# Optimization experiments

Hardware: AMD Instinct MI355X
Metric: run time of the kernel (lower is better)

The kernel has to match this reference:

```python
import jax, jax.numpy as jnp
import numpy as np
import math

D_MODEL = 1024
N_HEADS = 16
Q_PROJ = D_MODEL // 4
KV_PROJ = D_MODEL // 4
DH = D_MODEL // N_HEADS
LN_EPS = 1e-5


def _layernorm(x, gamma, beta):
    mu = jnp.mean(x, axis=-1, keepdims=True)
    var = jnp.mean(jnp.square(x - mu), axis=-1, keepdims=True)
    return (x - mu) * jax.lax.rsqrt(var + LN_EPS) * gamma + beta


def setup_inputs() -> dict:
    key = jax.random.key(0)
    ks = jax.random.split(key, 7)
    B, S = 2, 2048
    x = jax.random.normal(ks[0], (B, S, D_MODEL), dtype=jnp.float32)
    W_dq = 0.01 * jax.random.normal(ks[1], (D_MODEL, Q_PROJ), dtype=jnp.float32)
    W_uq = 0.01 * jax.random.normal(ks[2], (Q_PROJ, D_MODEL), dtype=jnp.float32)
    W_dkv = 0.01 * jax.random.normal(ks[3], (D_MODEL, KV_PROJ), dtype=jnp.float32)
    W_ukv = 0.01 * jax.random.normal(ks[4], (KV_PROJ, 2 * D_MODEL), dtype=jnp.float32)
    W_o = 0.01 * jax.random.normal(ks[5], (D_MODEL, D_MODEL), dtype=jnp.float32)
    return {
        "x": x,
        "W_dq": W_dq, "W_uq": W_uq,
        "q_ln_g": jnp.ones((Q_PROJ,), jnp.float32), "q_ln_b": jnp.zeros((Q_PROJ,), jnp.float32),
        "W_dkv": W_dkv, "W_ukv": W_ukv,
        "kv_ln_g": jnp.ones((KV_PROJ,), jnp.float32), "kv_ln_b": jnp.zeros((KV_PROJ,), jnp.float32),
        "W_o": W_o,
    }


def reference(x, W_dq, W_uq, q_ln_g, q_ln_b, W_dkv, W_ukv, kv_ln_g, kv_ln_b, W_o):
    B, S, D = x.shape
    # low-rank Q path
    cq = _layernorm(x @ W_dq, q_ln_g, q_ln_b)          # [B,S,q_proj]
    Q = cq @ W_uq                                       # [B,S,D]
    # low-rank KV path
    ckv = _layernorm(x @ W_dkv, kv_ln_g, kv_ln_b)       # [B,S,kv_proj]
    KV = ckv @ W_ukv                                    # [B,S,2D]
    K, V = KV[..., :D], KV[..., D:]
    q = Q.reshape(B, S, N_HEADS, DH)
    k = K.reshape(B, S, N_HEADS, DH)
    v = V.reshape(B, S, N_HEADS, DH)
    scores = jnp.einsum("bqhd,bkhd->bhqk", q, k) / math.sqrt(float(DH))
    # faithful to original: multiply by tril mask, then set exact zeros to -inf
    mask = jnp.tril(jnp.ones((S, S), dtype=scores.dtype))
    scores = scores * mask
    scores = jnp.where(scores == 0, -jnp.inf, scores)
    attn = jax.nn.softmax(scores, axis=-1)
    out = jnp.einsum("bhqk,bkhd->bqhd", attn, v).reshape(B, S, D)
    return out @ W_o.T
```

## Files before the change

kernel.cpp:

```cpp
#include <hip/hip_runtime.h>

typedef __bf16 bf16;
typedef __bf16 bf16x4 __attribute__((ext_vector_type(4)));
typedef __bf16 bf16x8 __attribute__((ext_vector_type(8)));
typedef float f32x4 __attribute__((ext_vector_type(4)));

#define D_MODEL 1024
#define PROJ    256
#define SEQ     2048
#define BATCH   2
#define TOK     4096
#define NH      16
#define DH      64
#define NEG_BIG (-1e30f)
#define QSCALE  0.18033688011112042f

#if __has_builtin(__builtin_amdgcn_exp2f)
#define EXP2(x) __builtin_amdgcn_exp2f(x)
#else
#define EXP2(x) exp2f(x)
#endif

typedef __attribute__((address_space(3))) unsigned int  lds_u32;
typedef __attribute__((address_space(1))) unsigned int  glb_u32;

__device__ __forceinline__ void gl2lds16(const void* gsrc, void* ldst) {
    __builtin_amdgcn_global_load_lds((const glb_u32*)gsrc, (lds_u32*)ldst, 16, 0, 0);
}

template <int CTRL>
__device__ __forceinline__ float dppmov(float x) {
    int i = __builtin_bit_cast(int, x);
    i = __builtin_amdgcn_update_dpp(i, i, CTRL, 0xf, 0xf, false);
    return __builtin_bit_cast(float, i);
}
__device__ __forceinline__ float rowsum16(float v) {
    v += dppmov<0xB1>(v);
    v += dppmov<0x4E>(v);
    v += dppmov<0x141>(v);
    v += dppmov<0x140>(v);
    return v;
}

__global__ __launch_bounds__(256) void prep_weights_kernel(
    const float* __restrict__ W_o, const float* __restrict__ x,
    bf16* __restrict__ Wo16, bf16* __restrict__ x16) {
    const int R0 = 1048576;
    const int R1 = R0 + 4194304;
    for (int i = blockIdx.x * blockDim.x + threadIdx.x; i < R1;
         i += gridDim.x * blockDim.x) {
        if (i < R0) Wo16[i] = (bf16)W_o[i];
        else        x16[i - R0] = (bf16)x[i - R0];
    }
}

__global__ __launch_bounds__(256) void transpose_cvt_kernel(
    const float* __restrict__ W_dq, const float* __restrict__ W_dkv,
    const float* __restrict__ W_uq, const float* __restrict__ W_ukv,
    bf16* __restrict__ Wt_dq, bf16* __restrict__ Wt_dkv,
    bf16* __restrict__ Wt_uq, bf16* __restrict__ Wt_ukv) {
    __shared__ float tile[64][65];
    const int m = blockIdx.y;
    const float* src; bf16* dst; int R, C;
    if (m == 0)      { src = W_dq;  dst = Wt_dq;  R = 1024; C = 256; }
    else if (m == 1) { src = W_dkv; dst = Wt_dkv; R = 1024; C = 256; }
    else if (m == 2) { src = W_uq;  dst = Wt_uq;  R = 256;  C = 1024; }
    else             { src = W_ukv; dst = Wt_ukv; R = 256;  C = 2048; }
    const int tilesC = C >> 6;
    const int ntile = (R >> 6) * tilesC;
    const int t = blockIdx.x;
    if (t >= ntile) return;
    const int r0 = (t / tilesC) << 6;
    const int c0 = (t % tilesC) << 6;
    const int tr = threadIdx.x >> 6;
    const int tc = threadIdx.x & 63;
#pragma unroll
    for (int i = 0; i < 16; ++i)
        tile[tr * 16 + i][tc] = src[(size_t)(r0 + tr * 16 + i) * C + c0 + tc];
    __syncthreads();
#pragma unroll
    for (int i = 0; i < 16; ++i)
        dst[(size_t)(c0 + tr * 16 + i) * R + r0 + tc] = (bf16)tile[tc][tr * 16 + i];
}

__global__ __launch_bounds__(256) void gemm_ln_kernel(
    const bf16* __restrict__ x16,
    const bf16* __restrict__ Wt_q, const bf16* __restrict__ Wt_kv,
    const float* __restrict__ q_g, const float* __restrict__ q_b,
    const float* __restrict__ kv_g, const float* __restrict__ kv_b,
    bf16* __restrict__ cq, bf16* __restrict__ ckv) {
    __shared__ alignas(16) bf16 xA[2][16 * 32];
    __shared__ alignas(16) bf16 wB[2][256 * 32];
    __shared__ float red1[4][16];
    __shared__ float red2[4][16];

    const int K = 1024;
    const bf16* Wt = blockIdx.y ? Wt_kv : Wt_q;
    const float* gamma = blockIdx.y ? kv_g : q_g;
    const float* beta  = blockIdx.y ? kv_b : q_b;
    bf16* out = blockIdx.y ? ckv : cq;

    const int m0 = blockIdx.x * 16;
    const int wv = threadIdx.x >> 6;
    const int lane = threadIdx.x & 63;
    const int g = lane >> 4;
    const int ln16 = lane & 15;

    const int crow = lane >> 2;
    const int ckc = lane & 3;
    const bf16* gx = x16 + (size_t)(m0 + crow) * K + ckc * 8;
    const bf16* gw = Wt + (size_t)(64 * wv + crow) * K + ckc * 8;

    f32x4 acc[4] = {};

    if (wv == 0) gl2lds16(gx, (char*)xA);
#pragma unroll
    for (int i = 0; i < 4; ++i)
        gl2lds16(gw + (size_t)i * 16 * K, (char*)wB + wv * 4096 + i * 1024);
    __syncthreads();

    int buf = 0;
    for (int k0 = 0; k0 < K; k0 += 32) {
        if (k0 + 32 < K) {
            const int nb = buf ^ 1;
            if (wv == 0) gl2lds16(gx + k0 + 32, (char*)xA + nb * 1024);
#pragma unroll
            for (int i = 0; i < 4; ++i)
                gl2lds16(gw + (size_t)i * 16 * K + k0 + 32,
                         (char*)wB + nb * 16384 + wv * 4096 + i * 1024);
        }
        const bf16* cx = &xA[buf][0];
        const bf16* cw = &wB[buf][0];
        bf16x8 a = *(const bf16x8*)(cx + ln16 * 32 + g * 8);
#pragma unroll
        for (int t = 0; t < 4; ++t) {
            bf16x8 b = *(const bf16x8*)(cw + (wv * 64 + 16 * t + ln16) * 32 + g * 8);
            acc[t] = __builtin_amdgcn_mfma_f32_16x16x32_bf16(a, b, acc[t], 0, 0, 0);
        }
        __syncthreads();
        buf ^= 1;
    }

    float s1[4], s2[4];
#pragma unroll
    for (int r = 0; r < 4; ++r) {
        float a = 0.f, b = 0.f;
#pragma unroll
        for (int t = 0; t < 4; ++t) { float v = acc[t][r]; a += v; b += v * v; }
        s1[r] = rowsum16(a); s2[r] = rowsum16(b);
    }
    if (ln16 == 0) {
#pragma unroll
        for (int r = 0; r < 4; ++r) {
            red1[wv][g * 4 + r] = s1[r];
            red2[wv][g * 4 + r] = s2[r];
        }
    }
    __syncthreads();
#pragma unroll
    for (int r = 0; r < 4; ++r) {
        int rl = g * 4 + r;
        float t1 = red1[0][rl] + red1[1][rl] + red1[2][rl] + red1[3][rl];
        float t2 = red2[0][rl] + red2[1][rl] + red2[2][rl] + red2[3][rl];
        float mu = t1 * (1.0f / 256.0f);
        float var = t2 * (1.0f / 256.0f) - mu * mu;
        float rs = rsqrtf(var + 1e-5f);
        int row = m0 + rl;
#pragma unroll
        for (int t = 0; t < 4; ++t) {
            int col = wv * 64 + 16 * t + ln16;
            float v = (acc[t][r] - mu) * rs * gamma[col] + beta[col];
            out[(size_t)row * PROJ + col] = (bf16)v;
        }
    }
}

template <typename OutT>
__device__ __forceinline__ void gemm_body(
    const bf16* __restrict__ A, const bf16* __restrict__ Bt,
    OutT* __restrict__ C, bf16* __restrict__ C2, int N, int K,
    int bx, int by, int mode, bf16* tA, bf16* tB) {
    const int w = threadIdx.x >> 6;
    const int lane = threadIdx.x & 63;
    const int g = lane >> 4;
    const int ln16 = lane & 15;
    const int wr = w >> 1;
    const int wc = w & 1;

    const int m0 = bx * 64;
    const int n0 = by * 128;

    const int crow = lane >> 2;
    const int ckc = lane & 3;
    const bf16* gA  = A  + (size_t)(m0 + w * 16 + crow) * K + ckc * 8;
    const bf16* gB0 = Bt + (size_t)(n0 + w * 16 + crow) * K + ckc * 8;
    const bf16* gB1 = Bt + (size_t)(n0 + 64 + w * 16 + crow) * K + ckc * 8;

    f32x4 acc[2][4] = {};

    gl2lds16(gA, (char*)tA + w * 1024);
    gl2lds16(gB0, (char*)tB + w * 1024);
    gl2lds16(gB1, (char*)tB + 4096 + w * 1024);
    __syncthreads();

    int buf = 0;
    for (int k0 = 0; k0 < K; k0 += 32) {
        if (k0 + 32 < K) {
            const int nb = buf ^ 1;
            gl2lds16(gA + k0 + 32, (char*)tA + nb * 4096 + w * 1024);
            gl2lds16(gB0 + k0 + 32, (char*)tB + nb * 8192 + w * 1024);
            gl2lds16(gB1 + k0 + 32, (char*)tB + nb * 8192 + 4096 + w * 1024);
        }
        const bf16* cA = tA + buf * 2048;
        const bf16* cB = tB + buf * 4096;

        bf16x8 af[2], bfr[4];
#pragma unroll
        for (int s = 0; s < 2; ++s)
            af[s] = *(const bf16x8*)(cA + (wr * 32 + s * 16 + ln16) * 32 + g * 8);
#pragma unroll
        for (int t = 0; t < 4; ++t)
            bfr[t] = *(const bf16x8*)(cB + (wc * 64 + t * 16 + ln16) * 32 + g * 8);
#pragma unroll
        for (int s = 0; s < 2; ++s)
#pragma unroll
            for (int t = 0; t < 4; ++t)
                acc[s][t] = __builtin_amdgcn_mfma_f32_16x16x32_bf16(
                    af[s], bfr[t], acc[s][t], 0, 0, 0);
        __syncthreads();
        buf ^= 1;
    }

#pragma unroll
    for (int s = 0; s < 2; ++s)
#pragma unroll
        for (int t = 0; t < 4; ++t) {
            const int col = n0 + wc * 64 + t * 16 + ln16;
            const int tok0 = m0 + wr * 32 + s * 16 + g * 4;
            if (mode == 2 && col >= 1024) {
                int cc = col - 1024;
                int h = cc >> 6, d = cc & 63;
                int b = tok0 >> 11, sq = tok0 & 2047;
                bf16x4 pk;
#pragma unroll
                for (int r = 0; r < 4; ++r) pk[r] = (bf16)acc[s][t][r];
                *(bf16x4*)(C2 + ((size_t)((b * 16 + h) * 64 + d) * SEQ + sq)) = pk;
            } else {
#pragma unroll
                for (int r = 0; r < 4; ++r) {
                    int row = tok0 + r;
                    float v = acc[s][t][r];
                    if (mode == 0) {
                        C[(size_t)row * N + col] = (OutT)v;
                    } else {
                        if (mode == 1) v *= QSCALE;
                        int h = col >> 6, d = col & 63;
                        int b = row >> 11, sq = row & 2047;
                        C[((size_t)((b * 16 + h) * 2048 + sq)) * 64 + d] = (OutT)v;
                    }
                }
            }
        }
}

__global__ __launch_bounds__(256) void gemm_o_kernel(
    const bf16* __restrict__ A, const bf16* __restrict__ Bt,
    float* __restrict__ C, int M, int N, int K) {
    __shared__ alignas(16) bf16 tA[2][64 * 32];
    __shared__ alignas(16) bf16 tB[2][128 * 32];
    gemm_body<float>(A, Bt, C, nullptr, N, K, blockIdx.x, blockIdx.y, 0,
                     &tA[0][0], &tB[0][0]);
}

__global__ __launch_bounds__(256) void gemm_qkv_kernel(
    const bf16* __restrict__ cq, const bf16* __restrict__ Wt_uq,
    const bf16* __restrict__ ckv, const bf16* __restrict__ Wt_ukv,
    bf16* __restrict__ Qh, bf16* __restrict__ Kh, bf16* __restrict__ Vt) {
    __shared__ alignas(16) bf16 tA[2][64 * 32];
    __shared__ alignas(16) bf16 tB[2][128 * 32];
    const int i = blockIdx.x;
    if (i < 512) {
        gemm_body<bf16>(cq, Wt_uq, Qh, nullptr, D_MODEL, PROJ,
                        i >> 3, i & 7, 1, &tA[0][0], &tB[0][0]);
    } else {
        const int j = i - 512;
        gemm_body<bf16>(ckv, Wt_ukv, Kh, Vt, 2 * D_MODEL, PROJ,
                        j >> 4, j & 15, 2, &tA[0][0], &tB[0][0]);
    }
}

__device__ __forceinline__ void qk_exp_pack(
    int k0, int q, bool masked, int g, int ln16,
    bf16x8 aq0, bf16x8 aq1, const bf16x8* Kf,
    bf16x8& P1, bf16x8& P2) {
    f32x4 sc[4];
    __builtin_amdgcn_s_setprio(1);
#pragma unroll
    for (int c = 0; c < 4; ++c) {
        f32x4 z = {};
        z = __builtin_amdgcn_mfma_f32_16x16x32_bf16(Kf[2 * c], aq0, z, 0, 0, 0);
        z = __builtin_amdgcn_mfma_f32_16x16x32_bf16(Kf[2 * c + 1], aq1, z, 0, 0, 0);
        sc[c] = z;
    }
    __builtin_amdgcn_s_setprio(0);
    if (masked) {
        const int kb = k0 + 8 * g;
#pragma unroll
        for (int c = 0; c < 4; ++c)
#pragma unroll
            for (int r = 0; r < 4; ++r) {
                int kcol = kb + (c & 1) * 4 + r + ((c >> 1) << 5);
                if (kcol > q) sc[c][r] = NEG_BIG;
            }
    }
#pragma unroll
    for (int c = 0; c < 4; ++c)
#pragma unroll
        for (int r = 0; r < 4; ++r) sc[c][r] = EXP2(sc[c][r]);
#pragma unroll
    for (int r = 0; r < 4; ++r) {
        P1[r] = (bf16)sc[0][r]; P1[4 + r] = (bf16)sc[1][r];
        P2[r] = (bf16)sc[2][r]; P2[4 + r] = (bf16)sc[3][r];
    }
}

__device__ __forceinline__ void pv_accum(
    bf16x8 P1, bf16x8 P2, const bf16x8* Vf, bf16x8 vones,
    f32x4* o, f32x4& oli) {
    __builtin_amdgcn_s_setprio(1);
#pragma unroll
    for (int t = 0; t < 4; ++t) {
        o[t] = __builtin_amdgcn_mfma_f32_16x16x32_bf16(Vf[2 * t], P1, o[t], 0, 0, 0);
        o[t] = __builtin_amdgcn_mfma_f32_16x16x32_bf16(Vf[2 * t + 1], P2, o[t], 0, 0, 0);
    }
    oli = __builtin_amdgcn_mfma_f32_16x16x32_bf16(vones, P1, oli, 0, 0, 0);
    oli = __builtin_amdgcn_mfma_f32_16x16x32_bf16(vones, P2, oli, 0, 0, 0);
    __builtin_amdgcn_s_setprio(0);
}

__global__ __launch_bounds__(256) void attn_kernel(
    const bf16* __restrict__ Qh, const bf16* __restrict__ Kh,
    const bf16* __restrict__ Vt, bf16* __restrict__ AT) {
    __shared__ alignas(128) bf16 kbuf[2][64 * 64];
    __shared__ alignas(128) bf16 vbuf[2][64 * 64];

    const int lane = threadIdx.x & 63;
    const int g = lane >> 4;
    const int ln16 = lane & 15;
    const int wv = threadIdx.x >> 6;

    const int bh = blockIdx.x & 31;
    const int qsuper = 31 - (blockIdx.x >> 5);
    const int nt = qsuper + 1;
    const int qb = qsuper * 64 + wv * 16;
    const int q = qb + ln16;

    const bf16* Kbh = Kh + (size_t)bh * SEQ * DH;
    const bf16* Vbh = Vt + (size_t)bh * DH * SEQ;

    const int rho = lane >> 3;
    const int sl  = lane & 7;
    int kofs[2];
    size_t vofs[2];
#pragma unroll
    for (int i = 0; i < 2; ++i) {
        const int row = 16 * wv + 8 * i + rho;
        const int c = sl ^ ((rho & 3) | ((i & 1) << 2));
        kofs[i] = row * 64 + c * 8;
        vofs[i] = (size_t)row * SEQ + c * 8;
    }

    const int row_base = ((ln16 & 12) << 1) + (ln16 & 3);
    int kro[4], vro[4];
#pragma unroll
    for (int c = 0; c < 4; ++c) {
        const int row = row_base + (c & 1) * 4 + ((c >> 1) << 5);
        const int fr = (row & 3) | (((row >> 3) & 1) << 2);
        kro[c] = row * 128 + (g ^ fr) * 16;
    }
#pragma unroll
    for (int t = 0; t < 4; ++t) {
        const int d = 16 * t + ln16;
        const int fd = (d & 3) | (((d >> 3) & 1) << 2);
        vro[t] = d * 128 + (g ^ fd) * 16;
    }

    const bf16* qp = Qh + ((size_t)bh * SEQ + q) * DH + g * 8;
    bf16x8 aq0 = *(const bf16x8*)qp, aq1 = *(const bf16x8*)(qp + 32);

    bf16x8 vones;
#pragma unroll
    for (int i = 0; i < 8; ++i) vones[i] = (bf16)1.0f;

    f32x4 o[4] = {};
    f32x4 oli = {};

#pragma unroll
    for (int i = 0; i < 2; ++i) {
        gl2lds16(Kbh + kofs[i], (char*)kbuf + wv * 2048 + i * 1024);
        gl2lds16(Vbh + vofs[i], (char*)vbuf + wv * 2048 + i * 1024);
    }
    __syncthreads();

    int cur = 0;
    for (int kt = 0; kt < nt; ++kt) {
        if (kt + 1 < nt) {
            const size_t k0n = (size_t)(kt + 1) * 64;
            char* kb = (char*)kbuf + (cur ^ 1) * 8192 + wv * 2048;
            char* vb = (char*)vbuf + (cur ^ 1) * 8192 + wv * 2048;
#pragma unroll
            for (int i = 0; i < 2; ++i) {
                gl2lds16(Kbh + k0n * 64 + kofs[i], kb + i * 1024);
                gl2lds16(Vbh + vofs[i] + k0n, vb + i * 1024);
            }
        }

        const char* kb = (const char*)kbuf + cur * 8192;
        const char* vb = (const char*)vbuf + cur * 8192;
        bf16x8 Kf[8], Vf[8];
#pragma unroll
        for (int c = 0; c < 4; ++c) {
            Kf[2 * c]     = *(const bf16x8*)(kb + kro[c]);
            Kf[2 * c + 1] = *(const bf16x8*)(kb + (kro[c] ^ 64));
        }
#pragma unroll
        for (int t = 0; t < 4; ++t) {
            Vf[2 * t]     = *(const bf16x8*)(vb + vro[t]);
            Vf[2 * t + 1] = *(const bf16x8*)(vb + (vro[t] ^ 64));
        }

        bf16x8 P1, P2;
        qk_exp_pack(kt * 64, q, kt == qsuper, g, ln16, aq0, aq1, Kf, P1, P2);
        pv_accum(P1, P2, Vf, vones, o, oli);
        __syncthreads();
        cur ^= 1;
    }

    const float inv = 1.0f / oli[0];
    const int b = bh >> 4, h = bh & 15;
    const size_t tok = (size_t)(b * SEQ + q) * D_MODEL + h * DH;
#pragma unroll
    for (int t = 0; t < 4; ++t) {
        bf16x4 pk;
#pragma unroll
        for (int r = 0; r < 4; ++r) pk[r] = (bf16)(o[t][r] * inv);
        *(bf16x4*)(AT + tok + 16 * t + 4 * g) = pk;
    }
}

extern "C" void kernel_launch(void* const* d_in, const int* in_sizes, int n_in,
                              void* d_out, int out_size, void* d_ws, size_t ws_size,
                              hipStream_t stream) {
    const float* x     = (const float*)d_in[0];
    const float* W_dq  = (const float*)d_in[1];
    const float* W_uq  = (const float*)d_in[2];
    const float* q_g   = (const float*)d_in[3];
    const float* q_b   = (const float*)d_in[4];
    const float* W_dkv = (const float*)d_in[5];
    const float* W_ukv = (const float*)d_in[6];
    const float* kv_g  = (const float*)d_in[7];
    const float* kv_b  = (const float*)d_in[8];
    const float* W_o   = (const float*)d_in[9];

    char* ws = (char*)d_ws;
    size_t off = 0;
    bf16* Wo16   = (bf16*)(ws + off); off += (size_t)D_MODEL * D_MODEL * 2;
    bf16* Wt_dq  = (bf16*)(ws + off); off += (size_t)PROJ * D_MODEL * 2;
    bf16* Wt_dkv = (bf16*)(ws + off); off += (size_t)PROJ * D_MODEL * 2;
    bf16* Wt_uq  = (bf16*)(ws + off); off += (size_t)D_MODEL * PROJ * 2;
    bf16* Wt_ukv = (bf16*)(ws + off); off += (size_t)(2 * D_MODEL) * PROJ * 2;
    bf16* x16    = (bf16*)(ws + off); off += (size_t)TOK * D_MODEL * 2;
    bf16* cq     = (bf16*)(ws + off); off += (size_t)TOK * PROJ * 2;
    bf16* ckv    = (bf16*)(ws + off); off += (size_t)TOK * PROJ * 2;
    bf16* Qh     = (bf16*)(ws + off); off += (size_t)TOK * D_MODEL * 2;
    bf16* Kh     = (bf16*)(ws + off); off += (size_t)TOK * D_MODEL * 2;
    bf16* Vt     = (bf16*)(ws + off); off += (size_t)TOK * D_MODEL * 2;
    bf16* AT     = (bf16*)(ws + off); off += (size_t)TOK * D_MODEL * 2;

    prep_weights_kernel<<<1024, 256, 0, stream>>>(W_o, x, Wo16, x16);

    transpose_cvt_kernel<<<dim3(128, 4), 256, 0, stream>>>(
        W_dq, W_dkv, W_uq, W_ukv, Wt_dq, Wt_dkv, Wt_uq, Wt_ukv);

    gemm_ln_kernel<<<dim3(TOK / 16, 2), 256, 0, stream>>>(
        x16, Wt_dq, Wt_dkv, q_g, q_b, kv_g, kv_b, cq, ckv);

    gemm_qkv_kernel<<<1536, 256, 0, stream>>>(cq, Wt_uq, ckv, Wt_ukv, Qh, Kh, Vt);

    attn_kernel<<<1024, 256, 0, stream>>>(Qh, Kh, Vt, AT);

    gemm_o_kernel<<<dim3(TOK / 64, D_MODEL / 128), 256, 0, stream>>>(
        AT, Wo16, (float*)d_out, TOK, D_MODEL, D_MODEL);
}
```

Baseline: 184.3 us.

## Merge prep kernels, enlarge QKV GEMM tiles, and give attention waves two query blocks

Fuses the conversion and transpose prep kernels into one launch and vectorizes the fp32-to-bf16 conversion with float4 loads. The QKV up-projection GEMM moves to 128x128 tiles, and the GEMM MFMA loops are wrapped in s_setprio. The attention kernel now runs 2 waves per block, each handling 32 query rows, so every K/V tile loaded into LDS is reused across two query blocks. The aim is fewer launches, more reuse per LDS load and less memory traffic, at the cost of higher register pressure and fewer waves per block in attention.

```diff
diff --git a/kernel.cpp b/kernel.cpp
--- a/kernel.cpp
+++ b/kernel.cpp
@@ -42,45 +42,55 @@
     return v;
 }
 
-__global__ __launch_bounds__(256) void prep_weights_kernel(
+__global__ __launch_bounds__(256) void prep_kernel(
     const float* __restrict__ W_o, const float* __restrict__ x,
-    bf16* __restrict__ Wo16, bf16* __restrict__ x16) {
-    const int R0 = 1048576;
-    const int R1 = R0 + 4194304;
-    for (int i = blockIdx.x * blockDim.x + threadIdx.x; i < R1;
-         i += gridDim.x * blockDim.x) {
-        if (i < R0) Wo16[i] = (bf16)W_o[i];
-        else        x16[i - R0] = (bf16)x[i - R0];
-    }
-}
-
-__global__ __launch_bounds__(256) void transpose_cvt_kernel(
     const float* __restrict__ W_dq, const float* __restrict__ W_dkv,
     const float* __restrict__ W_uq, const float* __restrict__ W_ukv,
+    bf16* __restrict__ Wo16, bf16* __restrict__ x16,
     bf16* __restrict__ Wt_dq, bf16* __restrict__ Wt_dkv,
     bf16* __restrict__ Wt_uq, bf16* __restrict__ Wt_ukv) {
-    __shared__ float tile[64][65];
-    const int m = blockIdx.y;
-    const float* src; bf16* dst; int R, C;
-    if (m == 0)      { src = W_dq;  dst = Wt_dq;  R = 1024; C = 256; }
-    else if (m == 1) { src = W_dkv; dst = Wt_dkv; R = 1024; C = 256; }
-    else if (m == 2) { src = W_uq;  dst = Wt_uq;  R = 256;  C = 1024; }
-    else             { src = W_ukv; dst = Wt_ukv; R = 256;  C = 2048; }
-    const int tilesC = C >> 6;
-    const int ntile = (R >> 6) * tilesC;
-    const int t = blockIdx.x;
-    if (t >= ntile) return;
-    const int r0 = (t / tilesC) << 6;
-    const int c0 = (t % tilesC) << 6;
-    const int tr = threadIdx.x >> 6;
-    const int tc = threadIdx.x & 63;
-#pragma unroll
-    for (int i = 0; i < 16; ++i)
-        tile[tr * 16 + i][tc] = src[(size_t)(r0 + tr * 16 + i) * C + c0 + tc];
-    __syncthreads();
-#pragma unroll
-    for (int i = 0; i < 16; ++i)
-        dst[(size_t)(c0 + tr * 16 + i) * R + r0 + tc] = (bf16)tile[tc][tr * 16 + i];
+    if (blockIdx.x < 320) {
+        __shared__ float tile[64][65];
+        int t = blockIdx.x;
+        const float* src; bf16* dst; int R, C;
+        if (t < 64)       { src = W_dq;  dst = Wt_dq;  R = 1024; C = 256; }
+        else if (t < 128) { src = W_dkv; dst = Wt_dkv; R = 1024; C = 256;  t -= 64; }
+        else if (t < 192) { src = W_uq;  dst = Wt_uq;  R = 256;  C = 1024; t -= 128; }
+        else              { src = W_ukv; dst = Wt_ukv; R = 256;  C = 2048; t -= 192; }
+        const int tilesC = C >> 6;
+        const int r0 = (t / tilesC) << 6;
+        const int c0 = (t % tilesC) << 6;
+        const int tr = threadIdx.x >> 6;
+        const int tc = threadIdx.x & 63;
+#pragma unroll
+        for (int i = 0; i < 16; ++i)
+            tile[tr * 16 + i][tc] = src[(size_t)(r0 + tr * 16 + i) * C + c0 + tc];
+        __syncthreads();
+#pragma unroll
+        for (int i = 0; i < 16; ++i)
+            dst[(size_t)(c0 + tr * 16 + i) * R + r0 + tc] =
+                (bf16)tile[tc][tr * 16 + i];
+    } else {
+        const int NW = 262144;
+        const int NX = 1048576;
+        for (int i = (blockIdx.x - 320) * 256 + threadIdx.x; i < NW + NX;
+             i += 1024 * 256) {
+            if (i < NW) {
+                float4 v = ((const float4*)W_o)[i];
+                bf16x4 p;
+                p[0] = (bf16)v.x; p[1] = (bf16)v.y;
+                p[2] = (bf16)v.z; p[3] = (bf16)v.w;
+                ((bf16x4*)Wo16)[i] = p;
+            } else {
+                int j = i - NW;
+                float4 v = ((const float4*)x)[j];
+                bf16x4 p;
+                p[0] = (bf16)v.x; p[1] = (bf16)v.y;
+                p[2] = (bf16)v.z; p[3] = (bf16)v.w;
+                ((bf16x4*)x16)[j] = p;
+            }
+        }
+    }
 }
 
 __global__ __launch_bounds__(256) void gemm_ln_kernel(
@@ -175,10 +185,9 @@
     }
 }
 
-template <typename OutT>
-__device__ __forceinline__ void gemm_body(
+__device__ __forceinline__ void gemm_body128(
     const bf16* __restrict__ A, const bf16* __restrict__ Bt,
-    OutT* __restrict__ C, bf16* __restrict__ C2, int N, int K,
+    bf16* __restrict__ C, bf16* __restrict__ C2, int K,
     int bx, int by, int mode, bf16* tA, bf16* tB) {
     const int w = threadIdx.x >> 6;
     const int lane = threadIdx.x & 63;
@@ -187,6 +196,111 @@
     const int wr = w >> 1;
     const int wc = w & 1;
 
+    const int m0 = bx * 128;
+    const int n0 = by * 128;
+
+    const int crow = lane >> 2;
+    const int ckc = lane & 3;
+    const bf16* gA0 = A  + (size_t)(m0 + 32 * w + crow) * K + ckc * 8;
+    const bf16* gA1 = gA0 + (size_t)16 * K;
+    const bf16* gB0 = Bt + (size_t)(n0 + 32 * w + crow) * K + ckc * 8;
+    const bf16* gB1 = gB0 + (size_t)16 * K;
+
+    f32x4 acc[4][4] = {};
+
+    gl2lds16(gA0, (char*)tA + w * 2048);
+    gl2lds16(gA1, (char*)tA + w * 2048 + 1024);
+    gl2lds16(gB0, (char*)tB + w * 2048);
+    gl2lds16(gB1, (char*)tB + w * 2048 + 1024);
+    __syncthreads();
+
+    int buf = 0;
+    for (int k0 = 0; k0 < K; k0 += 32) {
+        if (k0 + 32 < K) {
+            const int nb = buf ^ 1;
+            gl2lds16(gA0 + k0 + 32, (char*)tA + nb * 8192 + w * 2048);
+            gl2lds16(gA1 + k0 + 32, (char*)tA + nb * 8192 + w * 2048 + 1024);
+            gl2lds16(gB0 + k0 + 32, (char*)tB + nb * 8192 + w * 2048);
+            gl2lds16(gB1 + k0 + 32, (char*)tB + nb * 8192 + w * 2048 + 1024);
+        }
+        const bf16* cA = tA + buf * 4096;
+        const bf16* cB = tB + buf * 4096;
+
+        bf16x8 af[4], bfr[4];
+#pragma unroll
+        for (int s = 0; s < 4; ++s)
+            af[s] = *(const bf16x8*)(cA + (wr * 64 + s * 16 + ln16) * 32 + g * 8);
+#pragma unroll
+        for (int t = 0; t < 4; ++t)
+            bfr[t] = *(const bf16x8*)(cB + (wc * 64 + t * 16 + ln16) * 32 + g * 8);
+        __builtin_amdgcn_s_setprio(1);
+#pragma unroll
+        for (int s = 0; s < 4; ++s)
+#pragma unroll
+            for (int t = 0; t < 4; ++t)
+                acc[s][t] = __builtin_amdgcn_mfma_f32_16x16x32_bf16(
+                    af[s], bfr[t], acc[s][t], 0, 0, 0);
+        __builtin_amdgcn_s_setprio(0);
+        __syncthreads();
+        buf ^= 1;
+    }
+
+#pragma unroll
+    for (int s = 0; s < 4; ++s)
+#pragma unroll
+        for (int t = 0; t < 4; ++t) {
+            const int col = n0 + wc * 64 + t * 16 + ln16;
+            const int tok0 = m0 + wr * 64 + s * 16 + g * 4;
+            if (mode == 2 && col >= 1024) {
+                int cc = col - 1024;
+                int h = cc >> 6, d = cc & 63;
+                int b = tok0 >> 11, sq = tok0 & 2047;
+                bf16x4 pk;
+#pragma unroll
+                for (int r = 0; r < 4; ++r) pk[r] = (bf16)acc[s][t][r];
+                *(bf16x4*)(C2 + ((size_t)((b * 16 + h) * 64 + d) * SEQ + sq)) = pk;
+            } else {
+#pragma unroll
+                for (int r = 0; r < 4; ++r) {
+                    int row = tok0 + r;
+                    float v = acc[s][t][r];
+                    if (mode == 1) v *= QSCALE;
+                    int h = col >> 6, d = col & 63;
+                    int b = row >> 11, sq = row & 2047;
+                    C[((size_t)((b * 16 + h) * 2048 + sq)) * 64 + d] = (bf16)v;
+                }
+            }
+        }
+}
+
+__global__ __launch_bounds__(256) void gemm_qkv_kernel(
+    const bf16* __restrict__ cq, const bf16* __restrict__ Wt_uq,
+    const bf16* __restrict__ ckv, const bf16* __restrict__ Wt_ukv,
+    bf16* __restrict__ Qh, bf16* __restrict__ Kh, bf16* __restrict__ Vt) {
+    __shared__ alignas(16) bf16 tA[2][128 * 32];
+    __shared__ alignas(16) bf16 tB[2][128 * 32];
+    const int i = blockIdx.x;
+    if (i < 256) {
+        gemm_body128(cq, Wt_uq, Qh, nullptr, PROJ,
+                     i >> 3, i & 7, 1, &tA[0][0], &tB[0][0]);
+    } else {
+        const int j = i - 256;
+        gemm_body128(ckv, Wt_ukv, Kh, Vt, PROJ,
+                     j >> 4, j & 15, 2, &tA[0][0], &tB[0][0]);
+    }
+}
+
+__device__ __forceinline__ void gemm_body(
+    const bf16* __restrict__ A, const bf16* __restrict__ Bt,
+    float* __restrict__ C, int N, int K,
+    int bx, int by, bf16* tA, bf16* tB) {
+    const int w = threadIdx.x >> 6;
+    const int lane = threadIdx.x & 63;
+    const int g = lane >> 4;
+    const int ln16 = lane & 15;
+    const int wr = w >> 1;
+    const int wc = w & 1;
+
     const int m0 = bx * 64;
     const int n0 = by * 128;
 
@@ -221,12 +335,14 @@
 #pragma unroll
         for (int t = 0; t < 4; ++t)
             bfr[t] = *(const bf16x8*)(cB + (wc * 64 + t * 16 + ln16) * 32 + g * 8);
+        __builtin_amdgcn_s_setprio(1);
 #pragma unroll
         for (int s = 0; s < 2; ++s)
 #pragma unroll
             for (int t = 0; t < 4; ++t)
                 acc[s][t] = __builtin_amdgcn_mfma_f32_16x16x32_bf16(
                     af[s], bfr[t], acc[s][t], 0, 0, 0);
+        __builtin_amdgcn_s_setprio(0);
         __syncthreads();
         buf ^= 1;
     }
@@ -237,29 +353,9 @@
         for (int t = 0; t < 4; ++t) {
             const int col = n0 + wc * 64 + t * 16 + ln16;
             const int tok0 = m0 + wr * 32 + s * 16 + g * 4;
-            if (mode == 2 && col >= 1024) {
-                int cc = col - 1024;
-                int h = cc >> 6, d = cc & 63;
-                int b = tok0 >> 11, sq = tok0 & 2047;
-                bf16x4 pk;
-#pragma unroll
-                for (int r = 0; r < 4; ++r) pk[r] = (bf16)acc[s][t][r];
-                *(bf16x4*)(C2 + ((size_t)((b * 16 + h) * 64 + d) * SEQ + sq)) = pk;
-            } else {
-#pragma unroll
-                for (int r = 0; r < 4; ++r) {
-                    int row = tok0 + r;
-                    float v = acc[s][t][r];
-                    if (mode == 0) {
-                        C[(size_t)row * N + col] = (OutT)v;
-                    } else {
-                        if (mode == 1) v *= QSCALE;
-                        int h = col >> 6, d = col & 63;
-                        int b = row >> 11, sq = row & 2047;
-                        C[((size_t)((b * 16 + h) * 2048 + sq)) * 64 + d] = (OutT)v;
-                    }
-                }
-            }
+#pragma unroll
+            for (int r = 0; r < 4; ++r)
+                C[(size_t)(tok0 + r) * N + col] = acc[s][t][r];
         }
 }
 
@@ -268,25 +364,7 @@
     float* __restrict__ C, int M, int N, int K) {
     __shared__ alignas(16) bf16 tA[2][64 * 32];
     __shared__ alignas(16) bf16 tB[2][128 * 32];
-    gemm_body<float>(A, Bt, C, nullptr, N, K, blockIdx.x, blockIdx.y, 0,
-                     &tA[0][0], &tB[0][0]);
-}
-
-__global__ __launch_bounds__(256) void gemm_qkv_kernel(
-    const bf16* __restrict__ cq, const bf16* __restrict__ Wt_uq,
-    const bf16* __restrict__ ckv, const bf16* __restrict__ Wt_ukv,
-    bf16* __restrict__ Qh, bf16* __restrict__ Kh, bf16* __restrict__ Vt) {
-    __shared__ alignas(16) bf16 tA[2][64 * 32];
-    __shared__ alignas(16) bf16 tB[2][128 * 32];
-    const int i = blockIdx.x;
-    if (i < 512) {
-        gemm_body<bf16>(cq, Wt_uq, Qh, nullptr, D_MODEL, PROJ,
-                        i >> 3, i & 7, 1, &tA[0][0], &tB[0][0]);
-    } else {
-        const int j = i - 512;
-        gemm_body<bf16>(ckv, Wt_ukv, Kh, Vt, 2 * D_MODEL, PROJ,
-                        j >> 4, j & 15, 2, &tA[0][0], &tB[0][0]);
-    }
+    gemm_body(A, Bt, C, N, K, blockIdx.x, blockIdx.y, &tA[0][0], &tB[0][0]);
 }
 
 __device__ __forceinline__ void qk_exp_pack(
@@ -338,7 +416,7 @@
     __builtin_amdgcn_s_setprio(0);
 }
 
-__global__ __launch_bounds__(256) void attn_kernel(
+__global__ __launch_bounds__(128) void attn_kernel(
     const bf16* __restrict__ Qh, const bf16* __restrict__ Kh,
     const bf16* __restrict__ Vt, bf16* __restrict__ AT) {
     __shared__ alignas(128) bf16 kbuf[2][64 * 64];
@@ -352,19 +430,18 @@
     const int bh = blockIdx.x & 31;
     const int qsuper = 31 - (blockIdx.x >> 5);
     const int nt = qsuper + 1;
-    const int qb = qsuper * 64 + wv * 16;
-    const int q = qb + ln16;
+    const int qb = qsuper * 64 + wv * 32;
 
     const bf16* Kbh = Kh + (size_t)bh * SEQ * DH;
     const bf16* Vbh = Vt + (size_t)bh * DH * SEQ;
 
     const int rho = lane >> 3;
     const int sl  = lane & 7;
-    int kofs[2];
-    size_t vofs[2];
-#pragma unroll
-    for (int i = 0; i < 2; ++i) {
-        const int row = 16 * wv + 8 * i + rho;
+    int kofs[4];
+    size_t vofs[4];
+#pragma unroll
+    for (int i = 0; i < 4; ++i) {
+        const int row = 32 * wv + 8 * i + rho;
         const int c = sl ^ ((rho & 3) | ((i & 1) << 2));
         kofs[i] = row * 64 + c * 8;
         vofs[i] = (size_t)row * SEQ + c * 8;
@@ -385,20 +462,25 @@
         vro[t] = d * 128 + (g ^ fd) * 16;
     }
 
-    const bf16* qp = Qh + ((size_t)bh * SEQ + q) * DH + g * 8;
-    bf16x8 aq0 = *(const bf16x8*)qp, aq1 = *(const bf16x8*)(qp + 32);
+    bf16x8 aq[2][2];
+#pragma unroll
+    for (int hh = 0; hh < 2; ++hh) {
+        const bf16* qp = Qh + ((size_t)bh * SEQ + qb + 16 * hh + ln16) * DH + g * 8;
+        aq[hh][0] = *(const bf16x8*)qp;
+        aq[hh][1] = *(const bf16x8*)(qp + 32);
+    }
 
     bf16x8 vones;
 #pragma unroll
     for (int i = 0; i < 8; ++i) vones[i] = (bf16)1.0f;
 
-    f32x4 o[4] = {};
-    f32x4 oli = {};
-
-#pragma unroll
-    for (int i = 0; i < 2; ++i) {
-        gl2lds16(Kbh + kofs[i], (char*)kbuf + wv * 2048 + i * 1024);
-        gl2lds16(Vbh + vofs[i], (char*)vbuf + wv * 2048 + i * 1024);
+    f32x4 o0[4] = {}, o1[4] = {};
+    f32x4 oli0 = {}, oli1 = {};
+
+#pragma unroll
+    for (int i = 0; i < 4; ++i) {
+        gl2lds16(Kbh + kofs[i], (char*)kbuf + wv * 4096 + i * 1024);
+        gl2lds16(Vbh + vofs[i], (char*)vbuf + wv * 4096 + i * 1024);
     }
     __syncthreads();
 
@@ -406,10 +488,10 @@
     for (int kt = 0; kt < nt; ++kt) {
         if (kt + 1 < nt) {
             const size_t k0n = (size_t)(kt + 1) * 64;
-            char* kb = (char*)kbuf + (cur ^ 1) * 8192 + wv * 2048;
-            char* vb = (char*)vbuf + (cur ^ 1) * 8192 + wv * 2048;
-#pragma unroll
-            for (int i = 0; i < 2; ++i) {
+            char* kb = (char*)kbuf + (cur ^ 1) * 8192 + wv * 4096;
+            char* vb = (char*)vbuf + (cur ^ 1) * 8192 + wv * 4096;
+#pragma unroll
+            for (int i = 0; i < 4; ++i) {
                 gl2lds16(Kbh + k0n * 64 + kofs[i], kb + i * 1024);
                 gl2lds16(Vbh + vofs[i] + k0n, vb + i * 1024);
             }
@@ -429,22 +511,34 @@
             Vf[2 * t + 1] = *(const bf16x8*)(vb + (vro[t] ^ 64));
         }
 
-        bf16x8 P1, P2;
-        qk_exp_pack(kt * 64, q, kt == qsuper, g, ln16, aq0, aq1, Kf, P1, P2);
-        pv_accum(P1, P2, Vf, vones, o, oli);
+        const int k0 = kt * 64;
+        const bool msk = (kt == qsuper);
+        bf16x8 P1a, P2a, P1b, P2b;
+        qk_exp_pack(k0, qb + ln16, msk, g, ln16,
+                    aq[0][0], aq[0][1], Kf, P1a, P2a);
+        qk_exp_pack(k0, qb + 16 + ln16, msk, g, ln16,
+                    aq[1][0], aq[1][1], Kf, P1b, P2b);
+        pv_accum(P1a, P2a, Vf, vones, o0, oli0);
+        pv_accum(P1b, P2b, Vf, vones, o1, oli1);
         __syncthreads();
         cur ^= 1;
     }
 
-    const float inv = 1.0f / oli[0];
+    const float inv0 = 1.0f / oli0[0];
+    const float inv1 = 1.0f / oli1[0];
     const int b = bh >> 4, h = bh & 15;
-    const size_t tok = (size_t)(b * SEQ + q) * D_MODEL + h * DH;
+    const size_t tok0 = (size_t)(b * SEQ + qb + ln16) * D_MODEL + h * DH;
+    const size_t tok1 = (size_t)(b * SEQ + qb + 16 + ln16) * D_MODEL + h * DH;
 #pragma unroll
     for (int t = 0; t < 4; ++t) {
-        bf16x4 pk;
-#pragma unroll
-        for (int r = 0; r < 4; ++r) pk[r] = (bf16)(o[t][r] * inv);
-        *(bf16x4*)(AT + tok + 16 * t + 4 * g) = pk;
+        bf16x4 pk0, pk1;
+#pragma unroll
+        for (int r = 0; r < 4; ++r) {
+            pk0[r] = (bf16)(o0[t][r] * inv0);
+            pk1[r] = (bf16)(o1[t][r] * inv1);
+        }
+        *(bf16x4*)(AT + tok0 + 16 * t + 4 * g) = pk0;
+        *(bf16x4*)(AT + tok1 + 16 * t + 4 * g) = pk1;
     }
 }
 
@@ -477,17 +571,16 @@
     bf16* Vt     = (bf16*)(ws + off); off += (size_t)TOK * D_MODEL * 2;
     bf16* AT     = (bf16*)(ws + off); off += (size_t)TOK * D_MODEL * 2;
 
-    prep_weights_kernel<<<1024, 256, 0, stream>>>(W_o, x, Wo16, x16);
-
-    transpose_cvt_kernel<<<dim3(128, 4), 256, 0, stream>>>(
-        W_dq, W_dkv, W_uq, W_ukv, Wt_dq, Wt_dkv, Wt_uq, Wt_ukv);
+    prep_kernel<<<1344, 256, 0, stream>>>(
+        W_o, x, W_dq, W_dkv, W_uq, W_ukv,
+        Wo16, x16, Wt_dq, Wt_dkv, Wt_uq, Wt_ukv);
 
     gemm_ln_kernel<<<dim3(TOK / 16, 2), 256, 0, stream>>>(
         x16, Wt_dq, Wt_dkv, q_g, q_b, kv_g, kv_b, cq, ckv);
 
-    gemm_qkv_kernel<<<1536, 256, 0, stream>>>(cq, Wt_uq, ckv, Wt_ukv, Qh, Kh, Vt);
-
-    attn_kernel<<<1024, 256, 0, stream>>>(Qh, Kh, Vt, AT);
+    gemm_qkv_kernel<<<768, 256, 0, stream>>>(cq, Wt_uq, ckv, Wt_ukv, Qh, Kh, Vt);
+
+    attn_kernel<<<1024, 128, 0, stream>>>(Qh, Kh, Vt, AT);
 
     gemm_o_kernel<<<dim3(TOK / 64, D_MODEL / 128), 256, 0, stream>>>(
         AT, Wo16, (float*)d_out, TOK, D_MODEL, D_MODEL);
```

New measurement: 187.9 us. Within noise of the previous version (+2.0%).
